# Kernel optimization log

Measured on AMD Instinct MI355X. Metric: run time of the kernel, lower is better.

Reference implementation:

```python
import jax, jax.numpy as jnp
from jax import lax
import numpy as np

FEAT_STRIDE = 16
RATIOS = np.array([0.5, 1.0, 2.0])
SCALES = np.array([8.0, 16.0, 32.0])
PRE_NMS = 6000
POST_NMS = 300
NMS_THRESH = 0.7
MIN_SIZE = 16.0
A = 9  # num anchors per location


def _whctrs(a):
    w = a[2] - a[0] + 1.0
    h = a[3] - a[1] + 1.0
    return w, h, a[0] + 0.5 * (w - 1.0), a[1] + 0.5 * (h - 1.0)


def _mkanchors(ws, hs, cx, cy):
    return np.stack([cx - 0.5 * (ws - 1.0), cy - 0.5 * (hs - 1.0),
                     cx + 0.5 * (ws - 1.0), cy + 0.5 * (hs - 1.0)], axis=1)


def generate_anchors(base_size=16):
    base = np.array([1.0, 1.0, base_size, base_size]) - 1.0
    w, h, cx, cy = _whctrs(base)
    size = w * h
    ws = np.round(np.sqrt(size / RATIOS))
    hs = np.round(ws * RATIOS)
    ratio_anchors = _mkanchors(ws, hs, cx, cy)
    out = []
    for ra in ratio_anchors:
        w, h, cx, cy = _whctrs(ra)
        out.append(_mkanchors(w * SCALES, h * SCALES, cx, cy))
    return np.concatenate(out, axis=0).astype(np.float32)  # [9,4]


def setup_inputs() -> dict:
    key = jax.random.key(0)
    k1, k2 = jax.random.split(key)
    scores = jax.random.normal(k1, (1, 2 * A, 50, 80), dtype=jnp.float32)
    bbox_deltas = jax.random.normal(k2, (1, 4 * A, 50, 80), dtype=jnp.float32) * 0.5
    im_info = jnp.array([[800.0, 1280.0, 1.5]], dtype=jnp.float32)  # (h, w, scale)
    return {"scores": scores, "bbox_deltas": bbox_deltas, "im_info": im_info}


def reference(scores, bbox_deltas, im_info):
    base_anchors = jnp.asarray(generate_anchors())  # [A,4]
    H, W = scores.shape[-2], scores.shape[-1]

    # fg scores, flattened in (h, w, a) order to match anchor ordering
    sc = scores[:, A:, :, :].transpose(0, 2, 3, 1).reshape(-1)  # [K*A]

    # anchors for every feature-map location
    sx = (jnp.arange(W) * FEAT_STRIDE).astype(jnp.float32)
    sy = (jnp.arange(H) * FEAT_STRIDE).astype(jnp.float32)
    gy, gx = jnp.meshgrid(sy, sx, indexing="ij")
    shifts = jnp.stack([gx, gy, gx, gy], axis=-1).reshape(-1, 1, 4)  # [K,1,4]
    anchors = (base_anchors[None, :, :] + shifts).reshape(-1, 4)    # [K*A,4]

    # decode deltas (dw/dh clamped to [-10,10])
    d = bbox_deltas.transpose(0, 2, 3, 1).reshape(-1, 4)
    d = jnp.concatenate([d[:, :2], jnp.clip(d[:, 2:], -10.0, 10.0)], axis=1)
    aw = anchors[:, 2] - anchors[:, 0] + 1.0
    ah = anchors[:, 3] - anchors[:, 1] + 1.0
    acx = anchors[:, 0] + 0.5 * aw
    acy = anchors[:, 1] + 0.5 * ah
    pcx = d[:, 0] * aw + acx
    pcy = d[:, 1] * ah + acy
    pw = jnp.exp(d[:, 2]) * aw
    ph = jnp.exp(d[:, 3]) * ah
    boxes = jnp.stack([pcx - 0.5 * pw, pcy - 0.5 * ph,
                       pcx + 0.5 * pw, pcy + 0.5 * ph], axis=1)

    # clip to image
    im_h, im_w, im_s = im_info[0, 0], im_info[0, 1], im_info[0, 2]
    boxes = jnp.stack([
        jnp.clip(boxes[:, 0], 0.0, im_w - 1.0),
        jnp.clip(boxes[:, 1], 0.0, im_h - 1.0),
        jnp.clip(boxes[:, 2], 0.0, im_w - 1.0),
        jnp.clip(boxes[:, 3], 0.0, im_h - 1.0),
    ], axis=1)

    # min-size filter (masking instead of compaction, for static shapes)
    ws = boxes[:, 2] - boxes[:, 0] + 1.0
    hs = boxes[:, 3] - boxes[:, 1] + 1.0
    min_sz = MIN_SIZE * im_s
    valid = (ws >= min_sz) & (hs >= min_sz)
    sc = jnp.where(valid, sc, -jnp.inf)

    # pre-NMS top-k by score
    top_sc, top_idx = lax.top_k(sc, PRE_NMS)
    props = boxes[top_idx]  # [P,4], sorted by descending score
    alive0 = jnp.isfinite(top_sc)

    # pairwise IoU (the +1 pixel convention matching the rest of the pipeline)
    x1, y1, x2, y2 = props[:, 0], props[:, 1], props[:, 2], props[:, 3]
    areas = (x2 - x1 + 1.0) * (y2 - y1 + 1.0)
    iw = jnp.clip(jnp.minimum(x2[:, None], x2[None, :]) - jnp.maximum(x1[:, None], x1[None, :]) + 1.0, 0.0)
    ih = jnp.clip(jnp.minimum(y2[:, None], y2[None, :]) - jnp.maximum(y1[:, None], y1[None, :]) + 1.0, 0.0)
    inter = iw * ih
    iou = inter / (areas[:, None] + areas[None, :] - inter)  # [P,P] ~144MB

    idx = jnp.arange(PRE_NMS)

    def body(i, keep):
        sup = keep[i] & (iou[i] > NMS_THRESH) & (idx > i)
        return keep & ~sup

    keep = lax.fori_loop(0, PRE_NMS, body, alive0)

    # gather first POST_NMS kept proposals into fixed-size output [POST_NMS,5]
    rank = jnp.cumsum(keep) - 1
    dest = jnp.where(keep & (rank < POST_NMS), rank, POST_NMS)
    out = jnp.zeros((POST_NMS + 1, 5), dtype=scores.dtype)
    out = out.at[dest, 1:].set(props)
    return out[:POST_NMS]
```

## Files before the change

### kernel.cpp

```cpp
#include <hip/hip_runtime.h>
#include <stdint.h>

#define A_NUM 9
#define H_FM 50
#define W_FM 80
#define N_ANCH (A_NUM * H_FM * W_FM)
#define PRE_NMS_N 6000
#define POST_NMS_N 300
#define NMS_TH 0.7f
#define MASK_W 94
#define MASK_STRIDE 96
#define NBIN 4096
#define BIN_CAP 4096
#define NBD 141
#define MASK_TILES (24 * 94)

typedef unsigned long long ull;

struct ZeroRegion {
    int hist[NBIN];
    ull dead[MASK_STRIDE];
    ull rowany[MASK_STRIDE];
};

__constant__ float c_aw[9] = {184.f,368.f,736.f,128.f,256.f,512.f, 88.f,176.f,352.f};
__constant__ float c_ah[9] = { 96.f,192.f,384.f,128.f,256.f,512.f,176.f,352.f,704.f};

__device__ float4 g_boxes[N_ANCH];
__device__ float4 g_props[PRE_NMS_N];
__device__ ull    g_mask[(size_t)PRE_NMS_N * MASK_STRIDE];
__device__ ull    g_colsup[MASK_W * 64];

__global__ __launch_bounds__(256) void k_decode(const float* __restrict__ scores,
                                                const float* __restrict__ deltas,
                                                const float* __restrict__ iminfo,
                                                ZeroRegion* __restrict__ Z,
                                                ull* __restrict__ bins) {
    int i = blockIdx.x * 256 + threadIdx.x;
    if (i >= N_ANCH) return;

    int a    = i % A_NUM;
    int cell = i / A_NUM;
    int x    = cell % W_FM;
    int y    = cell / W_FM;
    const int hw = H_FM * W_FM;

    float sc = scores[(A_NUM + a) * hw + cell];

    int dbase = (a * 4) * hw + cell;
    float d0 = deltas[dbase];
    float d1 = deltas[dbase + hw];
    float d2 = deltas[dbase + 2 * hw];
    float d3 = deltas[dbase + 3 * hw];
    d2 = fminf(fmaxf(d2, -10.f), 10.f);
    d3 = fminf(fmaxf(d3, -10.f), 10.f);

    float aw = c_aw[a], ah = c_ah[a];
    float acx = (float)(x * 16 + 8);
    float acy = (float)(y * 16 + 8);

    float pcx = d0 * aw + acx;
    float pcy = d1 * ah + acy;
    float pw  = expf(d2) * aw;
    float ph  = expf(d3) * ah;

    float x1 = pcx - 0.5f * pw;
    float y1 = pcy - 0.5f * ph;
    float x2 = pcx + 0.5f * pw;
    float y2 = pcy + 0.5f * ph;

    float imh = iminfo[0], imw = iminfo[1], ims = iminfo[2];
    x1 = fminf(fmaxf(x1, 0.f), imw - 1.f);
    y1 = fminf(fmaxf(y1, 0.f), imh - 1.f);
    x2 = fminf(fmaxf(x2, 0.f), imw - 1.f);
    y2 = fminf(fmaxf(y2, 0.f), imh - 1.f);

    float wsz = x2 - x1 + 1.f;
    float hsz = y2 - y1 + 1.f;
    float minsz = 16.f * ims;
    bool valid = (wsz >= minsz) && (hsz >= minsz);

    g_boxes[i] = make_float4(x1, y1, x2, y2);

    unsigned int u   = __float_as_uint(sc);
    unsigned int asc = (u & 0x80000000u) ? ~u : (u | 0x80000000u);
    unsigned int dk  = ~asc;
    if (!valid) dk = 0xFF800000u;
    ull key = ((ull)dk << 32) | (unsigned int)i;

    int bin  = (int)(dk >> 20);
    int slot = atomicAdd(&Z->hist[bin], 1);
    if (slot < BIN_CAP) bins[(size_t)bin * BIN_CAP + slot] = key;
}

__global__ __launch_bounds__(256) void k_binsort(ZeroRegion* __restrict__ Z,
                                                 const ull* __restrict__ bins) {
    __shared__ ull sb[4096];
    __shared__ int red[256];
    int b = blockIdx.x;
    int cntf = Z->hist[b];
    if (cntf == 0) return;
    int tid = threadIdx.x;

    int part = 0;
    for (int j = tid; j < b; j += 256) part += Z->hist[j];
    red[tid] = part;
    __syncthreads();
    for (int off = 128; off > 0; off >>= 1) {
        if (tid < off) red[tid] += red[tid + off];
        __syncthreads();
    }
    int s0 = red[0];
    if (s0 >= PRE_NMS_N) return;

    int cnt = (cntf < BIN_CAP) ? cntf : BIN_CAP;
    const ull* seg = bins + (size_t)b * BIN_CAP;

    int P = 2; while (P < cnt) P <<= 1;
    for (int i = tid; i < P; i += 256) sb[i] = (i < cnt) ? seg[i] : ~0ULL;
    __syncthreads();
    for (int k2 = 2; k2 <= P; k2 <<= 1) {
        for (int j = k2 >> 1; j >= 1; j >>= 1) {
            for (int p = tid; p < (P >> 1); p += 256) {
                int i  = ((p & ~(j - 1)) << 1) | (p & (j - 1));
                int pr = i | j;
                bool up = ((i & k2) == 0);
                ull a = sb[i], c = sb[pr];
                if ((a > c) == up) { sb[i] = c; sb[pr] = a; }
            }
            __syncthreads();
        }
    }
    for (int i = tid; i < cnt; i += 256) {
        int r = s0 + i;
        if (r < PRE_NMS_N) {
            ull key = sb[i];
            unsigned int dk = (unsigned int)(key >> 32);
            if (dk < 0xFF800000u) {
                g_props[r] = g_boxes[(unsigned int)key];
            } else {
                g_props[r] = make_float4(0.f, 0.f, 0.f, 0.f);
                atomicOr(&Z->dead[r >> 6], 1ULL << (r & 63));
            }
        }
    }
}

__global__ __launch_bounds__(256) void k_maskcol(ZeroRegion* __restrict__ Z) {
    __shared__ float4 sj[256];
    int vb = blockIdx.x;
    int tid = threadIdx.x;

    if (vb < MASK_TILES) {
        int bx = vb % 24;
        int by = vb / 24;
        int jbase = bx * 256;
        int jj = jbase + tid;
        sj[tid] = (jj < PRE_NMS_N) ? g_props[jj] : make_float4(0.f, 0.f, 0.f, 0.f);
        __syncthreads();

        int li = tid & 63;
        int wl = tid >> 6;
        int i  = by * 64 + li;
        int w  = bx * 4 + wl;
        if (i >= PRE_NMS_N || w >= MASK_W) return;

        float4 bi = g_props[i];
        float ai = (bi.z - bi.x + 1.f) * (bi.w - bi.y + 1.f);
        ull bits = 0;
        int jstart = w * 64;
        int lbase = jstart - jbase;
        for (int b = 0; b < 64; ++b) {
            int j = jstart + b;
            if (j <= i || j >= PRE_NMS_N) continue;
            float4 bj = sj[lbase + b];
            float aj = (bj.z - bj.x + 1.f) * (bj.w - bj.y + 1.f);
            float iw = fminf(bi.z, bj.z) - fmaxf(bi.x, bj.x) + 1.f;
            float ih = fminf(bi.w, bj.w) - fmaxf(bi.y, bj.y) + 1.f;
            iw = fmaxf(iw, 0.f);
            ih = fmaxf(ih, 0.f);
            float inter = iw * ih;
            float iou = inter / (ai + aj - inter);
            if (iou > NMS_TH) bits |= (1ULL << b);
        }
        g_mask[(size_t)i * MASK_STRIDE + w] = bits;
        if (bits && w != (i >> 6)) atomicOr(&Z->rowany[i >> 6], 1ULL << (i & 63));
    } else {
        int w = vb - MASK_TILES;
        int gj = w * 64 + tid;
        if (tid < 64)
            sj[tid] = (gj < PRE_NMS_N) ? g_props[gj] : make_float4(0.f, 0.f, 0.f, 0.f);
        __syncthreads();
        if (tid < 64) {
            float4 bj = sj[tid];
            float aj = (bj.z - bj.x + 1.f) * (bj.w - bj.y + 1.f);
            ull bits = 0;
            for (int b = 0; b < tid; ++b) {
                float4 bi = sj[b];
                float ai = (bi.z - bi.x + 1.f) * (bi.w - bi.y + 1.f);
                float iw = fminf(bi.z, bj.z) - fmaxf(bi.x, bj.x) + 1.f;
                float ih = fminf(bi.w, bj.w) - fmaxf(bi.y, bj.y) + 1.f;
                iw = fmaxf(iw, 0.f);
                ih = fmaxf(ih, 0.f);
                float inter = iw * ih;
                float iou = inter / (ai + aj - inter);
                if (iou > NMS_TH) bits |= (1ULL << b);
            }
            g_colsup[gj] = bits;
        }
    }
}

#define BATCH 8
__global__ __launch_bounds__(256, 1) void k_scan(const ZeroRegion* __restrict__ Z,
                                                 float* __restrict__ out) {
    __shared__ ull scol[MASK_W * 64];
    __shared__ ull srow[MASK_W];
    __shared__ int s_kept[POST_NMS_N];
    __shared__ int s_kc;
    int tid = threadIdx.x;

    for (int i = tid; i < MASK_W * 64; i += 256) scol[i] = g_colsup[i];
    for (int i = tid; i < MASK_W; i += 256)      srow[i] = Z->rowany[i];
    __syncthreads();

    if (tid < 64) {
        int lane = tid;
        ull rm0 = Z->dead[lane];
        ull rm1 = (lane < MASK_W - 64) ? Z->dead[64 + lane] : ~0ULL;
        if (lane == 29) rm1 |= 0xFFFF000000000000ULL;
        int kc = 0;

        for (;;) {
            ull avail0 = __ballot(~rm0 != 0ULL);
            ull avail1 = __ballot(~rm1 != 0ULL);
            int w;
            if (avail0)      w = __ffsll(avail0) - 1;
            else if (avail1) w = 63 + __ffsll(avail1);
            else break;

            ull diag = scol[(w << 6) + lane];
            ull raw  = srow[w];
            ull curw = (w < 64) ? __shfl(rm0, w) : __shfl(rm1, w - 64);

            ull U = ~curw;
            ull K = 0;
            while (U) {
                ull UK = U | K;
                bool deadp = (diag & K)  != 0ULL;
                bool freep = (diag & UK) == 0ULL;
                ull nd = __ballot(deadp) & U;
                U &= ~nd;
                ull nk = __ballot(freep) & U;
                U &= ~nk;
                K |= nk;
                if (!nk && !nd) break;
            }

            int cnt  = __popcll(K);
            int take = min(cnt, POST_NMS_N - kc);
            if (K & (1ULL << lane)) {
                int pos = kc + __popcll(K & ((1ULL << lane) - 1ULL));
                if (pos < POST_NMS_N) s_kept[pos] = (w << 6) + lane;
            }
            kc += take;
            if (kc >= POST_NMS_N) break;

            if (w < 64) { if (lane == w)      rm0 = ~0ULL; }
            else        { if (lane == w - 64) rm1 = ~0ULL; }

            ull need = K & raw;
            while (need) {
                int id[BATCH];
                int n = 0;
#pragma unroll
                for (int t2 = 0; t2 < BATCH; ++t2) {
                    id[t2] = 0;
                    if (need) { id[t2] = __ffsll(need) - 1; need &= need - 1; n = t2 + 1; }
                }
                ull v0[BATCH], v1[BATCH];
#pragma unroll
                for (int t2 = 0; t2 < BATCH; ++t2) {
                    const ull* __restrict__ row =
                        g_mask + (size_t)((w << 6) + id[t2]) * MASK_STRIDE;
                    v0[t2] = row[lane];
                    v1[t2] = (lane < MASK_W - 64) ? row[64 + lane] : 0ULL;
                }
                ull a0 = 0, a1 = 0;
#pragma unroll
                for (int t2 = 0; t2 < BATCH; ++t2) {
                    ull m = (t2 < n) ? ~0ULL : 0ULL;
                    a0 |= v0[t2] & m;
                    a1 |= v1[t2] & m;
                }
                rm0 |= a0;
                rm1 |= a1;
            }
        }
        if (lane == 0) s_kc = (kc < POST_NMS_N) ? kc : POST_NMS_N;
    }
    __syncthreads();
    int kcf = s_kc;
    for (int r = tid; r < POST_NMS_N; r += 256) {
        float4 p = make_float4(0.f, 0.f, 0.f, 0.f);
        if (r < kcf) p = g_props[s_kept[r]];
        out[r * 5 + 0] = 0.f;
        out[r * 5 + 1] = p.x;
        out[r * 5 + 2] = p.y;
        out[r * 5 + 3] = p.z;
        out[r * 5 + 4] = p.w;
    }
}

extern "C" void kernel_launch(void* const* d_in, const int* in_sizes, int n_in,
                              void* d_out, int out_size, void* d_ws, size_t ws_size,
                              hipStream_t stream) {
    const float* scores = (const float*)d_in[0];
    const float* deltas = (const float*)d_in[1];
    const float* iminfo = (const float*)d_in[2];
    float* out = (float*)d_out;
    ZeroRegion* Z = (ZeroRegion*)d_ws;
    ull* bins = (ull*)((char*)d_ws + ((sizeof(ZeroRegion) + 255) & ~size_t(255)));

    hipMemsetAsync(Z, 0, sizeof(ZeroRegion), stream);
    k_decode<<<NBD, 256, 0, stream>>>(scores, deltas, iminfo, Z, bins);
    k_binsort<<<NBIN, 256, 0, stream>>>(Z, bins);
    k_maskcol<<<MASK_TILES + MASK_W, 256, 0, stream>>>(Z);
    k_scan<<<1, 256, 0, stream>>>(Z, out);
}
```

Baseline: 124.0 us.

## Skip lower-triangle IoU tiles and replace the memset with in-kernel resets

Mask tiles whose columns all lie at or below the row range now write zero mask words and return before any IoU work, which removes roughly half of the pairwise computation. The per-row inner loop starts and stops at the valid column bounds instead of testing every bit. The workspace memset is dropped. The histogram and the dead/rowany bitmaps move to device globals that later kernels clear for the next call. This depends on the globals starting at zero and on every call running the full pipeline.

```diff
diff --git a/kernel.cpp b/kernel.cpp
--- a/kernel.cpp
+++ b/kernel.cpp
@@ -17,15 +17,12 @@
 
 typedef unsigned long long ull;
 
-struct ZeroRegion {
-    int hist[NBIN];
-    ull dead[MASK_STRIDE];
-    ull rowany[MASK_STRIDE];
-};
-
 __constant__ float c_aw[9] = {184.f,368.f,736.f,128.f,256.f,512.f, 88.f,176.f,352.f};
 __constant__ float c_ah[9] = { 96.f,192.f,384.f,128.f,256.f,512.f,176.f,352.f,704.f};
 
+__device__ int    g_hist[NBIN];
+__device__ ull    g_dead[MASK_STRIDE];
+__device__ ull    g_rowany[MASK_STRIDE];
 __device__ float4 g_boxes[N_ANCH];
 __device__ float4 g_props[PRE_NMS_N];
 __device__ ull    g_mask[(size_t)PRE_NMS_N * MASK_STRIDE];
@@ -34,7 +31,6 @@
 __global__ __launch_bounds__(256) void k_decode(const float* __restrict__ scores,
                                                 const float* __restrict__ deltas,
                                                 const float* __restrict__ iminfo,
-                                                ZeroRegion* __restrict__ Z,
                                                 ull* __restrict__ bins) {
     int i = blockIdx.x * 256 + threadIdx.x;
     if (i >= N_ANCH) return;
@@ -89,21 +85,20 @@
     ull key = ((ull)dk << 32) | (unsigned int)i;
 
     int bin  = (int)(dk >> 20);
-    int slot = atomicAdd(&Z->hist[bin], 1);
+    int slot = atomicAdd(&g_hist[bin], 1);
     if (slot < BIN_CAP) bins[(size_t)bin * BIN_CAP + slot] = key;
 }
 
-__global__ __launch_bounds__(256) void k_binsort(ZeroRegion* __restrict__ Z,
-                                                 const ull* __restrict__ bins) {
+__global__ __launch_bounds__(256) void k_binsort(const ull* __restrict__ bins) {
     __shared__ ull sb[4096];
     __shared__ int red[256];
     int b = blockIdx.x;
-    int cntf = Z->hist[b];
+    int cntf = g_hist[b];
     if (cntf == 0) return;
     int tid = threadIdx.x;
 
     int part = 0;
-    for (int j = tid; j < b; j += 256) part += Z->hist[j];
+    for (int j = tid; j < b; j += 256) part += g_hist[j];
     red[tid] = part;
     __syncthreads();
     for (int off = 128; off > 0; off >>= 1) {
@@ -140,29 +135,39 @@
                 g_props[r] = g_boxes[(unsigned int)key];
             } else {
                 g_props[r] = make_float4(0.f, 0.f, 0.f, 0.f);
-                atomicOr(&Z->dead[r >> 6], 1ULL << (r & 63));
-            }
-        }
-    }
-}
-
-__global__ __launch_bounds__(256) void k_maskcol(ZeroRegion* __restrict__ Z) {
+                atomicOr(&g_dead[r >> 6], 1ULL << (r & 63));
+            }
+        }
+    }
+}
+
+__global__ __launch_bounds__(256) void k_maskcol() {
     __shared__ float4 sj[256];
     int vb = blockIdx.x;
     int tid = threadIdx.x;
 
+    if (vb < 16) g_hist[vb * 256 + tid] = 0;
+
     if (vb < MASK_TILES) {
         int bx = vb % 24;
         int by = vb / 24;
+
+        int li = tid & 63;
+        int wl = tid >> 6;
+        int i  = by * 64 + li;
+        int w  = bx * 4 + wl;
+
+        if (bx * 256 + 255 <= by * 64) {
+            if (i < PRE_NMS_N && w < MASK_W)
+                g_mask[(size_t)i * MASK_STRIDE + w] = 0ULL;
+            return;
+        }
+
         int jbase = bx * 256;
         int jj = jbase + tid;
         sj[tid] = (jj < PRE_NMS_N) ? g_props[jj] : make_float4(0.f, 0.f, 0.f, 0.f);
         __syncthreads();
 
-        int li = tid & 63;
-        int wl = tid >> 6;
-        int i  = by * 64 + li;
-        int w  = bx * 4 + wl;
         if (i >= PRE_NMS_N || w >= MASK_W) return;
 
         float4 bi = g_props[i];
@@ -170,9 +175,9 @@
         ull bits = 0;
         int jstart = w * 64;
         int lbase = jstart - jbase;
-        for (int b = 0; b < 64; ++b) {
-            int j = jstart + b;
-            if (j <= i || j >= PRE_NMS_N) continue;
+        int bstart = i + 1 - jstart; if (bstart < 0) bstart = 0;
+        int bend = PRE_NMS_N - jstart; if (bend > 64) bend = 64;
+        for (int b = bstart; b < bend; ++b) {
             float4 bj = sj[lbase + b];
             float aj = (bj.z - bj.x + 1.f) * (bj.w - bj.y + 1.f);
             float iw = fminf(bi.z, bj.z) - fmaxf(bi.x, bj.x) + 1.f;
@@ -184,7 +189,7 @@
             if (iou > NMS_TH) bits |= (1ULL << b);
         }
         g_mask[(size_t)i * MASK_STRIDE + w] = bits;
-        if (bits && w != (i >> 6)) atomicOr(&Z->rowany[i >> 6], 1ULL << (i & 63));
+        if (bits && w != (i >> 6)) atomicOr(&g_rowany[i >> 6], 1ULL << (i & 63));
     } else {
         int w = vb - MASK_TILES;
         int gj = w * 64 + tid;
@@ -212,8 +217,7 @@
 }
 
 #define BATCH 8
-__global__ __launch_bounds__(256, 1) void k_scan(const ZeroRegion* __restrict__ Z,
-                                                 float* __restrict__ out) {
+__global__ __launch_bounds__(256, 1) void k_scan(float* __restrict__ out) {
     __shared__ ull scol[MASK_W * 64];
     __shared__ ull srow[MASK_W];
     __shared__ int s_kept[POST_NMS_N];
@@ -221,13 +225,13 @@
     int tid = threadIdx.x;
 
     for (int i = tid; i < MASK_W * 64; i += 256) scol[i] = g_colsup[i];
-    for (int i = tid; i < MASK_W; i += 256)      srow[i] = Z->rowany[i];
+    for (int i = tid; i < MASK_W; i += 256)      srow[i] = g_rowany[i];
     __syncthreads();
 
     if (tid < 64) {
         int lane = tid;
-        ull rm0 = Z->dead[lane];
-        ull rm1 = (lane < MASK_W - 64) ? Z->dead[64 + lane] : ~0ULL;
+        ull rm0 = g_dead[lane];
+        ull rm1 = (lane < MASK_W - 64) ? g_dead[64 + lane] : ~0ULL;
         if (lane == 29) rm1 |= 0xFFFF000000000000ULL;
         int kc = 0;
 
@@ -300,6 +304,12 @@
         if (lane == 0) s_kc = (kc < POST_NMS_N) ? kc : POST_NMS_N;
     }
     __syncthreads();
+
+    for (int i = tid; i < MASK_STRIDE; i += 256) {
+        g_dead[i] = 0ULL;
+        g_rowany[i] = 0ULL;
+    }
+
     int kcf = s_kc;
     for (int r = tid; r < POST_NMS_N; r += 256) {
         float4 p = make_float4(0.f, 0.f, 0.f, 0.f);
@@ -319,12 +329,10 @@
     const float* deltas = (const float*)d_in[1];
     const float* iminfo = (const float*)d_in[2];
     float* out = (float*)d_out;
-    ZeroRegion* Z = (ZeroRegion*)d_ws;
-    ull* bins = (ull*)((char*)d_ws + ((sizeof(ZeroRegion) + 255) & ~size_t(255)));
-
-    hipMemsetAsync(Z, 0, sizeof(ZeroRegion), stream);
-    k_decode<<<NBD, 256, 0, stream>>>(scores, deltas, iminfo, Z, bins);
-    k_binsort<<<NBIN, 256, 0, stream>>>(Z, bins);
-    k_maskcol<<<MASK_TILES + MASK_W, 256, 0, stream>>>(Z);
-    k_scan<<<1, 256, 0, stream>>>(Z, out);
-}
+    ull* bins = (ull*)d_ws;
+
+    k_decode<<<NBD, 256, 0, stream>>>(scores, deltas, iminfo, bins);
+    k_binsort<<<NBIN, 256, 0, stream>>>(bins);
+    k_maskcol<<<MASK_TILES + MASK_W, 256, 0, stream>>>();
+    k_scan<<<1, 256, 0, stream>>>(out);
+}
```

New measurement: 118.0 us. -4.8%, faster.
